# Optimization experiments

Measured on AMD Instinct MI355X. Metric: run time of the kernel, lower is better.

The kernel has to match this reference:

```python
import jax, jax.numpy as jnp
import numpy as np

N = 20000          # nodes
E = 320000         # edges
C = 64             # channel multiplicity (64x0e node feats)
NATTR = 10         # node attr (species one-hot) dim
EDGE_FEAT = 8      # radial bessel features
L_DIMS = (1, 3, 5) # irrep dims for l = 0,1,2
RAD = [64, 64, 64]
AVG_NEIGH = 16.0
NUM_L = len(L_DIMS)


def setup_inputs() -> dict:
    key = jax.random.key(0)
    ks = jax.random.split(key, 12)
    node_attrs = jax.random.uniform(ks[0], (N, NATTR), dtype=jnp.float32)
    node_feats = jax.random.normal(ks[1], (N, C), dtype=jnp.float32)
    edge_attrs = jax.random.normal(ks[2], (E, sum(L_DIMS)), dtype=jnp.float32)
    edge_feats = jax.random.normal(ks[3], (E, EDGE_FEAT), dtype=jnp.float32)
    edge_index = jax.random.randint(ks[4], (2, E), 0, N, dtype=jnp.int64)
    # linear1: o3.Linear(64x0e -> 64x0e)
    W_lin1 = jax.random.normal(ks[5], (C, C), dtype=jnp.float32)
    # radial MLP: FullyConnectedNet([8,64,64,64,192], Identity)
    W_r0 = jax.random.normal(ks[6], (EDGE_FEAT, RAD[0]), dtype=jnp.float32)
    W_r1 = jax.random.normal(ks[7], (RAD[0], RAD[1]), dtype=jnp.float32)
    W_r2 = jax.random.normal(ks[8], (RAD[1], RAD[2]), dtype=jnp.float32)
    W_r3 = jax.random.normal(ks[9], (RAD[2], NUM_L * C), dtype=jnp.float32)
    # post-aggregation linear: o3.Linear(64x0e+64x1o+64x2e -> same), per-l 64x64 mix
    W_msg = jax.random.normal(ks[10], (NUM_L, C, C), dtype=jnp.float32)
    # skip_tp: FullyConnectedTensorProduct(64x0e, 10x0e -> 64x0e), 'uvw'
    W_skip = jax.random.normal(ks[11], (C, NATTR, C), dtype=jnp.float32)
    return {
        "node_attrs": node_attrs, "node_feats": node_feats,
        "edge_attrs": edge_attrs, "edge_feats": edge_feats,
        "edge_index": edge_index,
        "W_lin1": W_lin1, "W_r0": W_r0, "W_r1": W_r1, "W_r2": W_r2,
        "W_r3": W_r3, "W_msg": W_msg, "W_skip": W_skip,
    }


def reference(node_attrs, node_feats, edge_attrs, edge_feats, edge_index,
              W_lin1, W_r0, W_r1, W_r2, W_r3, W_msg, W_skip):
    sender, receiver = edge_index[0], edge_index[1]
    num_nodes = node_feats.shape[0]
    num_edges = edge_feats.shape[0]

    # linear1 (o3.Linear on scalars): fan_in normalized
    h = node_feats @ (W_lin1 / np.float32(np.sqrt(C)))           # [N, C]

    # radial MLP (e3nn FullyConnectedNet, identity activation)
    w = edge_feats
    for W in (W_r0, W_r1, W_r2, W_r3):
        w = w @ (W / np.float32(np.sqrt(W.shape[0])))
    tp_w = w.reshape(num_edges, NUM_L, C)                        # per-l 'uvu' weights

    # edge gather + weighted tensor product (0e x l -> l per channel)
    xs = h[sender]                                               # [E, C]
    blocks = []
    off = 0
    for l, d in enumerate(L_DIMS):
        y_l = edge_attrs[:, off:off + d]                         # [E, d]
        m_l = (xs * tp_w[:, l, :])[:, :, None] * y_l[:, None, :] # [E, C, d]
        blocks.append(m_l.reshape(num_edges, C * d))
        off += d
    mji = jnp.concatenate(blocks, axis=-1)                       # [E, C*9]

    # scatter-sum to receivers
    msg = jax.ops.segment_sum(mji, receiver, num_segments=num_nodes)  # [N, C*9]

    # per-l linear mix + avg-neighbor norm, then reshape_irreps -> [N, C, 9]
    out_blocks = []
    off = 0
    for l, d in enumerate(L_DIMS):
        m_l = msg[:, off:off + C * d].reshape(num_nodes, C, d)
        o_l = jnp.einsum('num,uv->nvm', m_l, W_msg[l]) / np.float32(np.sqrt(C))
        out_blocks.append(o_l)
        off += C * d
    out = jnp.concatenate(out_blocks, axis=-1) / np.float32(AVG_NEIGH)  # [N, C, 9]

    # self connection: FullyConnectedTensorProduct(64x0e, 10x0e -> 64x0e)
    sc = jnp.einsum('nu,nv,uvw->nw', h, node_attrs, W_skip) / np.float32(np.sqrt(C * NATTR))
    return out, sc
```

## Files before the change

kernel.cpp:

```cpp
#include <hip/hip_runtime.h>

#define N_NODES 20000
#define N_EDGES 320000
#define C 64
#define NATTR 10
#define MSG_DIM 576
#define WC_COLS 192
#define PRE 12
#define REC 20

__global__ __launch_bounds__(256) void node_linear_hist_skip(
        const float* __restrict__ nf,
        const float* __restrict__ W,
        float* __restrict__ h,
        const int* __restrict__ eidx,
        int* __restrict__ counts,
        const float* __restrict__ attrs,
        const float* __restrict__ Wskip,
        float* __restrict__ sc) {
    const int t = threadIdx.x;
    {
        const int e = blockIdx.x * 256 + t;
        atomicAdd(&counts[eidx[N_EDGES + e]], 1);
    }
    __shared__ __align__(16) float wbuf[5120];
    __shared__ float row[4][64];
    __shared__ float hl[16][64];
    const int lane = t & 63, wv = t >> 6;
    for (int i = t; i < 4096; i += 256) wbuf[i] = W[i] * 0.125f;
    __syncthreads();
    const int base = blockIdx.x * 16;
    #pragma unroll 1
    for (int it = 0; it < 4; ++it) {
        const int nl = it * 4 + wv;
        const int n = base + nl;
        row[wv][lane] = nf[(size_t)n * 64 + lane];
        float acc = 0.f;
        #pragma unroll
        for (int k = 0; k < 64; ++k) acc += row[wv][k] * wbuf[k * 64 + lane];
        h[(size_t)n * 64 + lane] = acc;
        hl[nl][lane] = acc;
    }

    float alr[4][NATTR];
    #pragma unroll
    for (int i = 0; i < 4; ++i) {
        const float* ap = attrs + (size_t)(base + wv + 4 * i) * NATTR;
        #pragma unroll
        for (int v = 0; v < NATTR; ++v) alr[i][v] = ap[v];
    }
    float acc4[4] = {0.f, 0.f, 0.f, 0.f};
    __syncthreads();

    #pragma unroll 1
    for (int ch = 0; ch < 8; ++ch) {
        const float4* src = reinterpret_cast<const float4*>(Wskip + ch * 5120);
        float4* dst = reinterpret_cast<float4*>(wbuf);
        #pragma unroll
        for (int i = 0; i < 5; ++i) dst[t + 256 * i] = src[t + 256 * i];
        __syncthreads();
        #pragma unroll 1
        for (int uu = 0; uu < 8; ++uu) {
            const int u = ch * 8 + uu;
            float tmp[4] = {0.f, 0.f, 0.f, 0.f};
            #pragma unroll
            for (int v = 0; v < NATTR; ++v) {
                const float wk = wbuf[(uu * NATTR + v) * 64 + lane];
                #pragma unroll
                for (int i = 0; i < 4; ++i) tmp[i] += alr[i][v] * wk;
            }
            #pragma unroll
            for (int i = 0; i < 4; ++i)
                acc4[i] += hl[wv + 4 * i][u] * tmp[i];
        }
        __syncthreads();
    }
    const float scale = 0.03952847075210474f;
    #pragma unroll
    for (int i = 0; i < 4; ++i)
        sc[(size_t)(base + wv + 4 * i) * 64 + lane] = acc4[i] * scale;
}

#define SCAN_PER 20
__global__ __launch_bounds__(1024) void scan_radial_kernel(
        const int* __restrict__ counts,
        int* __restrict__ start, int* __restrict__ cursor,
        const float* __restrict__ Wr0, const float* __restrict__ Wr1,
        const float* __restrict__ Wr2, const float* __restrict__ Wr3,
        float* __restrict__ Wc, float* __restrict__ rec) {
    __shared__ int wsum[16];
    __shared__ float T[8 * 64];
    __shared__ float T2[8 * 64];
    const int t = threadIdx.x, lane = t & 63, w = t >> 6;
    const float s0r = 0.35355339059327373f;
    const float s1r = 0.125f;

    const int base = t * SCAN_PER;
    int v[SCAN_PER];
    int s = 0;
    #pragma unroll
    for (int j = 0; j < SCAN_PER; ++j) {
        const int idx = base + j;
        v[j] = (idx < N_NODES) ? counts[idx] : 0;
        s += v[j];
    }
    int sc = s;
    #pragma unroll
    for (int off = 1; off < 64; off <<= 1) {
        int up = __shfl_up(sc, off);
        if (lane >= off) sc += up;
    }
    if (lane == 63) wsum[w] = sc;
    if (t < 16) rec[(size_t)(N_EDGES + t) * REC + 17] = 0.f;
    for (int i = t; i < 8 * 64; i += 1024) {
        int r = i >> 6, c2 = i & 63;
        float acc = 0.f;
        for (int k = 0; k < 64; ++k) acc += Wr0[r * 64 + k] * Wr1[k * 64 + c2];
        T[i] = acc * (s0r * s1r);
    }
    __syncthreads();
    if (t == 0) {
        int a = 0;
        #pragma unroll
        for (int i = 0; i < 16; ++i) { int x = wsum[i]; wsum[i] = a; a += x; }
    }
    for (int i = t; i < 8 * 64; i += 1024) {
        int r = i >> 6, c2 = i & 63;
        float acc = 0.f;
        for (int k = 0; k < 64; ++k) acc += T[r * 64 + k] * Wr2[k * 64 + c2];
        T2[i] = acc * s1r;
    }
    __syncthreads();
    int a = wsum[w] + (sc - s);
    #pragma unroll
    for (int j = 0; j < SCAN_PER; ++j) {
        const int idx = base + j;
        if (idx < N_NODES) {
            start[idx] = a;
            cursor[idx] = a;
            a += v[j];
        }
    }
    for (int i = t; i < 8 * WC_COLS; i += 1024) {
        int r = i / WC_COLS, c2 = i % WC_COLS;
        float acc = 0.f;
        for (int k = 0; k < 64; ++k) acc += T2[r * 64 + k] * Wr3[k * WC_COLS + c2];
        Wc[i] = acc * s1r;
    }
}

__global__ void scatter_build(const int* __restrict__ eidx,
                              const float* __restrict__ ef,
                              const float* __restrict__ ea,
                              int* __restrict__ cursor,
                              float* __restrict__ rec) {
    const int e = blockIdx.x * 256 + threadIdx.x;
    if (e >= N_EDGES) return;
    const int r = eidx[N_EDGES + e];
    const int s = eidx[e];
    const int pos = atomicAdd(&cursor[r], 1);
    const float4* f4 = reinterpret_cast<const float4*>(ef + (size_t)e * 8);
    const float* y = ea + (size_t)e * 9;
    float4* o = reinterpret_cast<float4*>(rec + (size_t)pos * REC);
    o[0] = f4[0];
    o[1] = f4[1];
    o[2] = make_float4(y[0], y[1], y[2], y[3]);
    o[3] = make_float4(y[4], y[5], y[6], y[7]);
    o[4] = make_float4(y[8], __int_as_float(s), 0.f, 0.f);
}

__global__ __launch_bounds__(256) void gather_sorted(
                              const float* __restrict__ rec,
                              const float* __restrict__ h,
                              const float* __restrict__ Wc,
                              const int* __restrict__ start,
                              const int* __restrict__ counts,
                              float* __restrict__ msg) {
    __shared__ float part[2][9][64];
    __shared__ __align__(16) float erec[4][PRE * REC];
    const int t = threadIdx.x, lane = t & 63, wv = t >> 6;
    const int g = wv >> 1;
    const int half = wv & 1;
    const int n = blockIdx.x * 2 + g;

    float wc0[8], wc1[8], wc2[8];
    #pragma unroll
    for (int k = 0; k < 8; ++k) {
        wc0[k] = Wc[k * WC_COLS + lane];
        wc1[k] = Wc[k * WC_COLS + 64 + lane];
        wc2[k] = Wc[k * WC_COLS + 128 + lane];
    }

    const int s0 = start[n], cnt = counts[n];
    const int jbeg = half ? (cnt >> 1) : 0;
    const int jend = half ? cnt : (cnt >> 1);
    const int m = jend - jbeg;
    const int base = s0 + jbeg;

    if (lane < PRE * REC / 4) {
        const float4 v = *reinterpret_cast<const float4*>(
            rec + (size_t)base * REC + lane * 4);
        *reinterpret_cast<float4*>(&erec[wv][lane * 4]) = v;
    }
    __syncthreads();

    float p0 = 0.f;
    float p1[3] = {0.f, 0.f, 0.f};
    float p2[5] = {0.f, 0.f, 0.f, 0.f, 0.f};

    const int P = (m < PRE) ? m : PRE;
    int snd[PRE];
    #pragma unroll
    for (int b = 0; b < PRE; ++b) snd[b] = __float_as_int(erec[wv][b * REC + 17]);
    float xs[PRE];
    #pragma unroll
    for (int b = 0; b < PRE; ++b) {
        const int sb = (b < P) ? snd[b] : snd[0];
        xs[b] = h[(size_t)sb * 64 + lane];
    }

    #pragma unroll
    for (int j = 0; j < PRE; ++j) {
        if (j < P) {
            const float* er = &erec[wv][j * REC];
            const float4 e0 = *reinterpret_cast<const float4*>(er);
            const float4 e1 = *reinterpret_cast<const float4*>(er + 4);
            const float4 ya = *reinterpret_cast<const float4*>(er + 8);
            const float4 yb = *reinterpret_cast<const float4*>(er + 12);
            const float  y8 = er[16];
            const float* fk = reinterpret_cast<const float*>(&e0);
            const float* gk = reinterpret_cast<const float*>(&e1);
            float w0 = fk[0] * wc0[0], w1 = fk[0] * wc1[0], w2 = fk[0] * wc2[0];
            #pragma unroll
            for (int k = 1; k < 4; ++k) {
                w0 += fk[k] * wc0[k]; w1 += fk[k] * wc1[k]; w2 += fk[k] * wc2[k];
            }
            #pragma unroll
            for (int k = 0; k < 4; ++k) {
                w0 += gk[k] * wc0[k + 4]; w1 += gk[k] * wc1[k + 4]; w2 += gk[k] * wc2[k + 4];
            }
            const float b0 = xs[j] * w0, b1 = xs[j] * w1, b2 = xs[j] * w2;
            p0    += b0 * ya.x;
            p1[0] += b1 * ya.y; p1[1] += b1 * ya.z; p1[2] += b1 * ya.w;
            p2[0] += b2 * yb.x; p2[1] += b2 * yb.y; p2[2] += b2 * yb.z;
            p2[3] += b2 * yb.w; p2[4] += b2 * y8;
        }
    }
    for (int j = PRE; j < m; ++j) {
        const float4* q = reinterpret_cast<const float4*>(rec + (size_t)(base + j) * REC);
        const float4 fa = q[0], fb = q[1];
        const float4 ya = q[2], yb = q[3], yc = q[4];
        const int snd_t = __float_as_int(yc.y);
        const float xs_t = h[(size_t)snd_t * 64 + lane];
        const float* fk = reinterpret_cast<const float*>(&fa);
        const float* gk = reinterpret_cast<const float*>(&fb);
        float w0 = fk[0] * wc0[0], w1 = fk[0] * wc1[0], w2 = fk[0] * wc2[0];
        #pragma unroll
        for (int k = 1; k < 4; ++k) {
            w0 += fk[k] * wc0[k]; w1 += fk[k] * wc1[k]; w2 += fk[k] * wc2[k];
        }
        #pragma unroll
        for (int k = 0; k < 4; ++k) {
            w0 += gk[k] * wc0[k + 4]; w1 += gk[k] * wc1[k + 4]; w2 += gk[k] * wc2[k + 4];
        }
        const float b0 = xs_t * w0, b1 = xs_t * w1, b2 = xs_t * w2;
        p0    += b0 * ya.x;
        p1[0] += b1 * ya.y; p1[1] += b1 * ya.z; p1[2] += b1 * ya.w;
        p2[0] += b2 * yb.x; p2[1] += b2 * yb.y; p2[2] += b2 * yb.z;
        p2[3] += b2 * yb.w; p2[4] += b2 * yc.x;
    }

    if (half) {
        part[g][0][lane] = p0;
        #pragma unroll
        for (int m2 = 0; m2 < 3; ++m2) part[g][1 + m2][lane] = p1[m2];
        #pragma unroll
        for (int m2 = 0; m2 < 5; ++m2) part[g][4 + m2][lane] = p2[m2];
    }
    __syncthreads();
    if (!half) {
        float* mrow = msg + (size_t)n * MSG_DIM;
        mrow[lane] = p0 + part[g][0][lane];
        #pragma unroll
        for (int m2 = 0; m2 < 3; ++m2)
            mrow[64 + lane * 3 + m2] = p1[m2] + part[g][1 + m2][lane];
        #pragma unroll
        for (int m2 = 0; m2 < 5; ++m2)
            mrow[256 + lane * 5 + m2] = p2[m2] + part[g][4 + m2][lane];
    }
}

__global__ __launch_bounds__(256) void out_transform(
        const float* __restrict__ Wmsg,
        float* __restrict__ out) {
    __shared__ __align__(16) float stage[16 * MSG_DIM];
    const int t = threadIdx.x, lane = t & 63, wv = t >> 6;
    {
        const float4* src = reinterpret_cast<const float4*>(
            out + (size_t)blockIdx.x * 16 * MSG_DIM);
        float4* dst = reinterpret_cast<float4*>(stage);
        #pragma unroll
        for (int i = 0; i < 9; ++i) dst[t + 256 * i] = src[t + 256 * i];
    }
    __syncthreads();
    const float scale = 1.f / 128.f;

    const int r0 = wv * 4;
    float o[4][9] = {};
    #pragma unroll 1
    for (int c = 0; c < 16; ++c) {
        const int u0 = c * 4;
        float w0[4], w1[4], w2[4];
        #pragma unroll
        for (int k = 0; k < 4; ++k) {
            w0[k] = Wmsg[(u0 + k) * 64 + lane];
            w1[k] = Wmsg[4096 + (u0 + k) * 64 + lane];
            w2[k] = Wmsg[8192 + (u0 + k) * 64 + lane];
        }
        #pragma unroll
        for (int rr = 0; rr < 4; ++rr) {
            const float* row = stage + (size_t)(r0 + rr) * MSG_DIM;
            float* o9 = o[rr];
            const float4 c0 = *reinterpret_cast<const float4*>(row + u0);
            const float4 c1a = *reinterpret_cast<const float4*>(row + 64 + u0 * 3);
            const float4 c1b = *reinterpret_cast<const float4*>(row + 64 + u0 * 3 + 4);
            const float4 c1c = *reinterpret_cast<const float4*>(row + 64 + u0 * 3 + 8);
            const float4 c2a = *reinterpret_cast<const float4*>(row + 256 + u0 * 5);
            const float4 c2b = *reinterpret_cast<const float4*>(row + 256 + u0 * 5 + 4);
            const float4 c2c = *reinterpret_cast<const float4*>(row + 256 + u0 * 5 + 8);
            const float4 c2d = *reinterpret_cast<const float4*>(row + 256 + u0 * 5 + 12);
            const float4 c2e = *reinterpret_cast<const float4*>(row + 256 + u0 * 5 + 16);
            o9[0] += c0.x * w0[0] + c0.y * w0[1] + c0.z * w0[2] + c0.w * w0[3];
            o9[1] += c1a.x * w1[0] + c1a.w * w1[1] + c1b.z * w1[2] + c1c.y * w1[3];
            o9[2] += c1a.y * w1[0] + c1b.x * w1[1] + c1b.w * w1[2] + c1c.z * w1[3];
            o9[3] += c1a.z * w1[0] + c1b.y * w1[1] + c1c.x * w1[2] + c1c.w * w1[3];
            o9[4] += c2a.x * w2[0] + c2b.y * w2[1] + c2c.z * w2[2] + c2d.w * w2[3];
            o9[5] += c2a.y * w2[0] + c2b.z * w2[1] + c2c.w * w2[2] + c2e.x * w2[3];
            o9[6] += c2a.z * w2[0] + c2b.w * w2[1] + c2d.x * w2[2] + c2e.y * w2[3];
            o9[7] += c2a.w * w2[0] + c2c.x * w2[1] + c2d.y * w2[2] + c2e.z * w2[3];
            o9[8] += c2b.x * w2[0] + c2c.y * w2[1] + c2d.z * w2[2] + c2e.w * w2[3];
        }
    }
    #pragma unroll
    for (int rr = 0; rr < 4; ++rr) {
        float* op = out + ((size_t)blockIdx.x * 16 + r0 + rr) * MSG_DIM + lane * 9;
        #pragma unroll
        for (int m = 0; m < 9; ++m) op[m] = o[rr][m] * scale;
    }
}

extern "C" void kernel_launch(void* const* d_in, const int* in_sizes, int n_in,
                              void* d_out, int out_size, void* d_ws, size_t ws_size,
                              hipStream_t stream) {
    const float* node_attrs = (const float*)d_in[0];
    const float* node_feats = (const float*)d_in[1];
    const float* edge_attrs = (const float*)d_in[2];
    const float* edge_feats = (const float*)d_in[3];
    const int*   edge_index = (const int*)d_in[4];
    const float* W_lin1 = (const float*)d_in[5];
    const float* W_r0 = (const float*)d_in[6];
    const float* W_r1 = (const float*)d_in[7];
    const float* W_r2 = (const float*)d_in[8];
    const float* W_r3 = (const float*)d_in[9];
    const float* W_msg = (const float*)d_in[10];
    const float* W_skip = (const float*)d_in[11];

    float* out = (float*)d_out;
    float* sc  = out + (size_t)N_NODES * MSG_DIM;

    float* wsf = (float*)d_ws;
    float* Wc = wsf;
    float* h  = wsf + 2048;
    int* wsi   = (int*)(wsf + 2048 + (size_t)N_NODES * 64);
    int* counts = wsi;
    int* start  = wsi + N_NODES;
    int* cursor = wsi + 2 * N_NODES;
    float* rec  = (float*)(wsi + 3 * N_NODES);

    hipMemsetAsync(counts, 0, N_NODES * sizeof(int), stream);
    node_linear_hist_skip<<<1250, 256, 0, stream>>>(node_feats, W_lin1, h,
                                                    edge_index, counts,
                                                    node_attrs, W_skip, sc);
    scan_radial_kernel<<<1, 1024, 0, stream>>>(counts, start, cursor,
                                               W_r0, W_r1, W_r2, W_r3, Wc, rec);
    scatter_build<<<1250, 256, 0, stream>>>(
        edge_index, edge_feats, edge_attrs, cursor, rec);
    gather_sorted<<<N_NODES / 2, 256, 0, stream>>>(
        rec, h, Wc, start, counts, out);
    out_transform<<<1250, 256, 0, stream>>>(W_msg, out);
}
```

Before: 223.0 us.

## Split fused node kernel into histogram, linear, and deferred skip kernels

Breaks the fused histogram/linear/skip-TP kernel into three kernels: a standalone edge histogram, a node linear, and a skip tensor-product kernel launched later, after the gather. The skip kernel now handles 32 nodes per block instead of 16, so each staged W_skip chunk is reused across twice as many nodes. The aim is to take the heavy skip work off the critical path ahead of the single-block scan and to cut W_skip reloads. The cost is extra launches, a reread of h from global memory, and more registers per thread in the skip kernel.

```diff
diff --git a/kernel.cpp b/kernel.cpp
--- a/kernel.cpp
+++ b/kernel.cpp
@@ -9,76 +9,86 @@
 #define PRE 12
 #define REC 20
 
-__global__ __launch_bounds__(256) void node_linear_hist_skip(
+__global__ void hist_kernel(const int* __restrict__ eidx, int* __restrict__ counts) {
+    const int e = blockIdx.x * 256 + threadIdx.x;
+    if (e < N_EDGES) atomicAdd(&counts[eidx[N_EDGES + e]], 1);
+}
+
+__global__ __launch_bounds__(256) void node_linear(
         const float* __restrict__ nf,
         const float* __restrict__ W,
-        float* __restrict__ h,
-        const int* __restrict__ eidx,
-        int* __restrict__ counts,
+        float* __restrict__ h) {
+    __shared__ float Ws[64 * 64];
+    __shared__ float row[4][64];
+    const int t = threadIdx.x, lane = t & 63, wv = t >> 6;
+    for (int i = t; i < 4096; i += 256) Ws[i] = W[i] * 0.125f;
+    __syncthreads();
+    const int base = blockIdx.x * 16;
+    #pragma unroll 1
+    for (int it = 0; it < 4; ++it) {
+        const int n = base + it * 4 + wv;
+        row[wv][lane] = nf[(size_t)n * 64 + lane];
+        float acc = 0.f;
+        #pragma unroll
+        for (int k = 0; k < 64; ++k) acc += row[wv][k] * Ws[k * 64 + lane];
+        h[(size_t)n * 64 + lane] = acc;
+    }
+}
+
+__global__ __launch_bounds__(256) void skip_kernel(
+        const float* __restrict__ h,
         const float* __restrict__ attrs,
         const float* __restrict__ Wskip,
         float* __restrict__ sc) {
-    const int t = threadIdx.x;
+    __shared__ __align__(16) float hl[32 * 64];
+    __shared__ __align__(16) float wch[5120];
+    const int t = threadIdx.x, lane = t & 63, wv = t >> 6;
+    const int base = blockIdx.x * 32;
     {
-        const int e = blockIdx.x * 256 + t;
-        atomicAdd(&counts[eidx[N_EDGES + e]], 1);
-    }
-    __shared__ __align__(16) float wbuf[5120];
-    __shared__ float row[4][64];
-    __shared__ float hl[16][64];
-    const int lane = t & 63, wv = t >> 6;
-    for (int i = t; i < 4096; i += 256) wbuf[i] = W[i] * 0.125f;
-    __syncthreads();
-    const int base = blockIdx.x * 16;
-    #pragma unroll 1
-    for (int it = 0; it < 4; ++it) {
-        const int nl = it * 4 + wv;
-        const int n = base + nl;
-        row[wv][lane] = nf[(size_t)n * 64 + lane];
-        float acc = 0.f;
-        #pragma unroll
-        for (int k = 0; k < 64; ++k) acc += row[wv][k] * wbuf[k * 64 + lane];
-        h[(size_t)n * 64 + lane] = acc;
-        hl[nl][lane] = acc;
-    }
-
-    float alr[4][NATTR];
-    #pragma unroll
-    for (int i = 0; i < 4; ++i) {
+        const float4* src = reinterpret_cast<const float4*>(h + (size_t)base * 64);
+        float4* dst = reinterpret_cast<float4*>(hl);
+        #pragma unroll
+        for (int i = 0; i < 2; ++i) dst[t + 256 * i] = src[t + 256 * i];
+    }
+    float alr[8][NATTR];
+    #pragma unroll
+    for (int i = 0; i < 8; ++i) {
         const float* ap = attrs + (size_t)(base + wv + 4 * i) * NATTR;
         #pragma unroll
         for (int v = 0; v < NATTR; ++v) alr[i][v] = ap[v];
     }
-    float acc4[4] = {0.f, 0.f, 0.f, 0.f};
+    float acc[8] = {0.f, 0.f, 0.f, 0.f, 0.f, 0.f, 0.f, 0.f};
     __syncthreads();
 
     #pragma unroll 1
     for (int ch = 0; ch < 8; ++ch) {
-        const float4* src = reinterpret_cast<const float4*>(Wskip + ch * 5120);
-        float4* dst = reinterpret_cast<float4*>(wbuf);
-        #pragma unroll
-        for (int i = 0; i < 5; ++i) dst[t + 256 * i] = src[t + 256 * i];
+        {
+            const float4* src = reinterpret_cast<const float4*>(Wskip + ch * 5120);
+            float4* dst = reinterpret_cast<float4*>(wch);
+            #pragma unroll
+            for (int i = 0; i < 5; ++i) dst[t + 256 * i] = src[t + 256 * i];
+        }
         __syncthreads();
         #pragma unroll 1
         for (int uu = 0; uu < 8; ++uu) {
             const int u = ch * 8 + uu;
-            float tmp[4] = {0.f, 0.f, 0.f, 0.f};
+            float tmp[8] = {0.f, 0.f, 0.f, 0.f, 0.f, 0.f, 0.f, 0.f};
             #pragma unroll
             for (int v = 0; v < NATTR; ++v) {
-                const float wk = wbuf[(uu * NATTR + v) * 64 + lane];
+                const float wk = wch[(uu * NATTR + v) * 64 + lane];
                 #pragma unroll
-                for (int i = 0; i < 4; ++i) tmp[i] += alr[i][v] * wk;
+                for (int i = 0; i < 8; ++i) tmp[i] += alr[i][v] * wk;
             }
             #pragma unroll
-            for (int i = 0; i < 4; ++i)
-                acc4[i] += hl[wv + 4 * i][u] * tmp[i];
+            for (int i = 0; i < 8; ++i)
+                acc[i] += hl[(wv + 4 * i) * 64 + u] * tmp[i];
         }
         __syncthreads();
     }
     const float scale = 0.03952847075210474f;
     #pragma unroll
-    for (int i = 0; i < 4; ++i)
-        sc[(size_t)(base + wv + 4 * i) * 64 + lane] = acc4[i] * scale;
+    for (int i = 0; i < 8; ++i)
+        sc[(size_t)(base + wv + 4 * i) * 64 + lane] = acc[i] * scale;
 }
 
 #define SCAN_PER 20
@@ -378,14 +388,14 @@
     float* rec  = (float*)(wsi + 3 * N_NODES);
 
     hipMemsetAsync(counts, 0, N_NODES * sizeof(int), stream);
-    node_linear_hist_skip<<<1250, 256, 0, stream>>>(node_feats, W_lin1, h,
-                                                    edge_index, counts,
-                                                    node_attrs, W_skip, sc);
+    hist_kernel<<<1250, 256, 0, stream>>>(edge_index, counts);
+    node_linear<<<1250, 256, 0, stream>>>(node_feats, W_lin1, h);
     scan_radial_kernel<<<1, 1024, 0, stream>>>(counts, start, cursor,
                                                W_r0, W_r1, W_r2, W_r3, Wc, rec);
     scatter_build<<<1250, 256, 0, stream>>>(
         edge_index, edge_feats, edge_attrs, cursor, rec);
     gather_sorted<<<N_NODES / 2, 256, 0, stream>>>(
         rec, h, Wc, start, counts, out);
+    skip_kernel<<<625, 256, 0, stream>>>(h, node_attrs, W_skip, sc);
     out_transform<<<1250, 256, 0, stream>>>(W_msg, out);
 }
```

After: 227.5 us. 2.0% more time.
